# Kernel optimization log

Measured on AMD Instinct MI355X. Metric: run time of the kernel, lower is better.

## Reference

```python
import jax, jax.numpy as jnp
import numpy as np

B, S, DIN, DQ, DK = 8, 2048, 1024, 64, 64

def setup_inputs() -> dict:
    key = jax.random.key(0)
    ks = jax.random.split(key, 8)
    sc = 0.02
    return {
        "input_tensor": jax.random.normal(ks[0], (B, S, DIN), jnp.float32),
        "attention_mask": jax.random.randint(ks[1], (B, 1, S), 0, 2) == 1,
        "Wq": jax.random.normal(ks[2], (DIN, DQ), jnp.float32) * sc,
        "bq": jnp.zeros((DQ,), jnp.float32),
        "Wk": jax.random.normal(ks[3], (DIN, DK), jnp.float32) * sc,
        "bk": jnp.zeros((DK,), jnp.float32),
        "Wv": jax.random.normal(ks[4], (DIN, DK), jnp.float32) * sc,
        "bv": jnp.zeros((DK,), jnp.float32),
    }

def reference(input_tensor, attention_mask, Wq, bq, Wk, bk, Wv, bv):
    q = input_tensor @ Wq + bq          # [B,S,DQ]
    k = input_tensor @ Wk + bk          # [B,S,DK]
    v = input_tensor @ Wv + bv          # [B,S,DK]
    # NOTE: original scales by sqrt(query.size(1)) == sqrt(seq_len), faithfully kept
    scale = q.shape[1] ** 0.5
    scores = jnp.einsum('bqd,bkd->bqk', q, k) / scale
    scores = jnp.where(attention_mask, jnp.float32(-1e9), scores)
    attn = jax.nn.softmax(scores, axis=-1)
    context = jnp.einsum('bqk,bkd->bqd', attn, v)
    return context
```

## Files before the change

kernel.cpp:

```cpp
#include <hip/hip_runtime.h>
#include <hip/hip_bf16.h>

#define NB 8
#define SEQ 2048
#define DIN 1024
#define DH 64

typedef __attribute__((ext_vector_type(8))) short bf16x8;
typedef __attribute__((ext_vector_type(4))) float f32x4;

static __device__ __forceinline__ unsigned short f2bf(float f) {
    unsigned int u = __builtin_bit_cast(unsigned int, f);
    unsigned int r = (u + 0x7FFFu + ((u >> 16) & 1u)) >> 16;
    return (unsigned short)r;
}

static __device__ __forceinline__ unsigned int cvt_pk_bf16(float lo, float hi) {
    unsigned int d;
    asm volatile("v_cvt_pk_bf16_f32 %0, %1, %2" : "=v"(d) : "v"(lo), "v"(hi));
    return d;
}

__global__ __launch_bounds__(256) void prep_kernel(
    const float* __restrict__ Wq, const float* __restrict__ Wk, const float* __restrict__ Wv,
    unsigned short* __restrict__ Wfrag)
{
    int j = blockIdx.x * 256 + threadIdx.x;
    int mat = j >> 16;
    int rem = j & 65535;
    int k = rem >> 6;
    int c = rem & 63;
    const float* W = (mat == 0) ? Wq : ((mat == 1) ? Wk : Wv);
    float v = W[rem];
    int col = mat * 64 + c;
    int cg = col >> 4, cl = col & 15;
    int kk = k >> 5, kq = (k >> 3) & 3, ke = k & 7;
    Wfrag[(size_t)(cg * 32 + kk) * 512 + cl * 32 + kq * 8 + ke] = f2bf(v);
}

__global__ __launch_bounds__(256, 2) void qkv_kernel(
    const float* __restrict__ X, const unsigned short* __restrict__ Wfrag,
    const float* __restrict__ bq, const float* __restrict__ bk, const float* __restrict__ bv,
    unsigned short* __restrict__ Qb, unsigned short* __restrict__ Kb, unsigned short* __restrict__ Vt)
{
    __shared__ __align__(16) short As[2][32][128];

    const int tid = threadIdx.x;
    const int w   = tid >> 6;
    const int l15 = tid & 15;
    const int lq  = (tid >> 4) & 3;
    const int row0 = blockIdx.x * 32;

    f32x4 acc[2][3] = {};

    const float* xb = X + (size_t)row0 * DIN;

    const unsigned short* wfb[3];
    #pragma unroll
    for (int n = 0; n < 3; ++n)
        wfb[n] = Wfrag + (size_t)((w * 3 + n) * 32) * 512 + (l15 * 4 + lq) * 8;

    float4 pf[2][4];
    #pragma unroll
    for (int i = 0; i < 4; ++i) {
        int c = tid + 256 * i;
        const float* p = xb + (size_t)(c >> 5) * DIN + (c & 31) * 4;
        pf[0][i] = *(const float4*)(p);
        pf[1][i] = *(const float4*)(p + 128);
    }

    bf16x8 wb[6][3];
    #pragma unroll
    for (int s = 0; s < 6; ++s)
        #pragma unroll
        for (int n = 0; n < 3; ++n)
            wb[s][n] = *(const bf16x8*)(wfb[n] + (size_t)s * 512);

    #pragma unroll
    for (int step = 0; step < 8; ++step) {
        const int pi = step & 1;

        unsigned int u[8];
        #pragma unroll
        for (int i = 0; i < 4; ++i) {
            u[2 * i]     = cvt_pk_bf16(pf[pi][i].x, pf[pi][i].y);
            u[2 * i + 1] = cvt_pk_bf16(pf[pi][i].z, pf[pi][i].w);
        }
        #pragma unroll
        for (int i = 0; i < 4; ++i) {
            int c = tid + 256 * i;
            int r = c >> 5;
            int bo = ((c & 31) * 8) ^ ((r & 7) << 4);
            uint2 v2; v2.x = u[2 * i]; v2.y = u[2 * i + 1];
            *(uint2*)((char*)&As[pi][r][0] + bo) = v2;
        }
        if (step + 2 < 8) {
            #pragma unroll
            for (int i = 0; i < 4; ++i) {
                int c = tid + 256 * i;
                pf[pi][i] = *(const float4*)(xb + (size_t)(c >> 5) * DIN + (step + 2) * 128 + (c & 31) * 4);
            }
        }
        __syncthreads();

        #pragma unroll
        for (int kkl = 0; kkl < 4; ++kkl) {
            const int c = step * 4 + kkl;
            bf16x8 a[2];
            #pragma unroll
            for (int m = 0; m < 2; ++m) {
                int r = m * 16 + l15;
                int bo = ((kkl * 32 + lq * 8) * 2) ^ ((r & 7) << 4);
                a[m] = *(const bf16x8*)((const char*)&As[pi][r][0] + bo);
            }
            #pragma unroll
            for (int m = 0; m < 2; ++m)
                #pragma unroll
                for (int n = 0; n < 3; ++n)
                    acc[m][n] = __builtin_amdgcn_mfma_f32_16x16x32_bf16(a[m], wb[c % 6][n], acc[m][n], 0, 0, 0);
            if (c + 6 < 32) {
                #pragma unroll
                for (int n = 0; n < 3; ++n)
                    wb[c % 6][n] = *(const bf16x8*)(wfb[n] + (size_t)(c + 6) * 512);
            }
        }
    }

    #pragma unroll
    for (int n = 0; n < 3; ++n) {
        int col = w * 48 + n * 16 + l15;
        int mat = col >> 6, c = col & 63;
        float badd = ((mat == 0) ? bq : ((mat == 1) ? bk : bv))[c];
        #pragma unroll
        for (int m = 0; m < 2; ++m) {
            #pragma unroll
            for (int reg = 0; reg < 4; ++reg) {
                int row = row0 + m * 16 + lq * 4 + reg;
                unsigned short v16 = f2bf(acc[m][n][reg] + badd);
                if (mat == 0)      Qb[(size_t)row * DH + c] = v16;
                else if (mat == 1) Kb[(size_t)row * DH + c] = v16;
                else {
                    int bb = row >> 11, ss = row & 2047;
                    Vt[((size_t)(bb * DH + c)) * SEQ + ss] = v16;
                }
            }
        }
    }
}

#define AKT 64
#define ANT 8
#define PP 36

__global__ __launch_bounds__(256, 3) void attn_kernel(
    const unsigned short* __restrict__ Qb, const unsigned short* __restrict__ Kb,
    const unsigned short* __restrict__ Vt, const int* __restrict__ mask,
    float* __restrict__ Opart, float* __restrict__ lpart)
{
    __shared__ __align__(16) short Ks[2][AKT][DH];
    __shared__ __align__(16) short Vs[2][DH][AKT];
    __shared__ __align__(16) short ps[4][32][PP];
    __shared__ float sml[4][32];

    const int tid = threadIdx.x;
    const int w   = tid >> 6;
    const int l15 = tid & 15;
    const int lq  = (tid >> 4) & 3;
    const int wm  = w >> 1;
    const int wn  = w & 1;

    int bid = blockIdx.x;
    int sbid = (bid & 7) * 128 + (bid >> 3);
    const int b   = sbid >> 7;
    const int qt  = (sbid >> 2) & 31;
    const int kq  = sbid & 3;
    const int q0  = qt * 64;
    const int kb0 = kq * 512;

    bf16x8 aq[2][2];
    #pragma unroll
    for (int m = 0; m < 2; ++m)
        #pragma unroll
        for (int kk = 0; kk < 2; ++kk)
            aq[m][kk] = *(const bf16x8*)(Qb + ((size_t)(b * SEQ + q0 + wm * 32 + m * 16 + l15)) * DH + kk * 32 + lq * 8);

    const int srow = tid >> 3;
    const int scol = (tid & 7) * 8;
    const int sdst = scol ^ ((srow & 7) << 3);

    const unsigned short* Kst = Kb + ((size_t)(b * SEQ) + kb0 + srow) * DH + scol;
    const unsigned short* Vst = Vt + ((size_t)(b * DH) + srow) * SEQ + kb0 + scol;

    bf16x8 kr[2], vr[2];
    #pragma unroll
    for (int i = 0; i < 2; ++i) {
        kr[i] = *(const bf16x8*)(Kst + (size_t)(i * 32) * DH);
        vr[i] = *(const bf16x8*)(Vst + (size_t)(i * 32) * SEQ);
    }

    f32x4 o[2][4];
    #pragma unroll
    for (int m = 0; m < 2; ++m)
        #pragma unroll
        for (int n = 0; n < 4; ++n) o[m][n] = f32x4{0, 0, 0, 0};
    float lr[2][4] = {};

    const float rscale = 0.022097086912079612f;
    const int* mbase = mask + b * SEQ + kb0 + wn * 32 + l15;

    for (int t = 0; t < ANT; ++t) {
        const int cur = t & 1;

        #pragma unroll
        for (int i = 0; i < 2; ++i) *(bf16x8*)&Ks[cur][i * 32 + srow][sdst] = kr[i];
        #pragma unroll
        for (int i = 0; i < 2; ++i) *(bf16x8*)&Vs[cur][i * 32 + srow][sdst] = vr[i];

        int mk0 = mbase[t * AKT];
        int mk1 = mbase[t * AKT + 16];

        if (t + 1 < ANT) {
            #pragma unroll
            for (int i = 0; i < 2; ++i) {
                kr[i] = *(const bf16x8*)(Kst + (size_t)((t + 1) * AKT + i * 32) * DH);
                vr[i] = *(const bf16x8*)(Vst + (size_t)(i * 32) * SEQ + (t + 1) * AKT);
            }
        }

        __syncthreads();

        bf16x8 bkf[2][2];
        #pragma unroll
        for (int n = 0; n < 2; ++n)
            #pragma unroll
            for (int kk = 0; kk < 2; ++kk) {
                int row = wn * 32 + n * 16 + l15;
                bkf[n][kk] = *(const bf16x8*)&Ks[cur][row][(kk * 32 + lq * 8) ^ ((row & 7) << 3)];
            }
        f32x4 s[2][2];
        #pragma unroll
        for (int m = 0; m < 2; ++m)
            #pragma unroll
            for (int n = 0; n < 2; ++n) s[m][n] = f32x4{0, 0, 0, 0};
        #pragma unroll
        for (int kk = 0; kk < 2; ++kk)
            #pragma unroll
            for (int m = 0; m < 2; ++m)
                #pragma unroll
                for (int n = 0; n < 2; ++n)
                    s[m][n] = __builtin_amdgcn_mfma_f32_16x16x32_bf16(aq[m][kk], bkf[n][kk], s[m][n], 0, 0, 0);

        float bb0 = mk0 ? -1e30f : 0.0f;
        float bb1 = mk1 ? -1e30f : 0.0f;
        #pragma unroll
        for (int m = 0; m < 2; ++m)
            #pragma unroll
            for (int n = 0; n < 2; ++n) {
                float bvv = n ? bb1 : bb0;
                #pragma unroll
                for (int r = 0; r < 4; ++r) {
                    float p = __expf(fmaf(s[m][n][r], rscale, bvv));
                    lr[m][r] += p;
                    ps[w][m * 16 + lq * 4 + r][n * 16 + l15] = (short)f2bf(p);
                }
            }

        bf16x8 pa[2];
        #pragma unroll
        for (int m = 0; m < 2; ++m)
            pa[m] = *(const bf16x8*)&ps[w][m * 16 + l15][lq * 8];
        bf16x8 bvf[4];
        #pragma unroll
        for (int n = 0; n < 4; ++n) {
            int row = n * 16 + l15;
            bvf[n] = *(const bf16x8*)&Vs[cur][row][(wn * 32 + lq * 8) ^ ((row & 7) << 3)];
        }
        #pragma unroll
        for (int m = 0; m < 2; ++m)
            #pragma unroll
            for (int n = 0; n < 4; ++n)
                o[m][n] = __builtin_amdgcn_mfma_f32_16x16x32_bf16(pa[m], bvf[n], o[m][n], 0, 0, 0);
    }

    #pragma unroll
    for (int off = 1; off < 16; off <<= 1)
        #pragma unroll
        for (int m = 0; m < 2; ++m)
            #pragma unroll
            for (int r = 0; r < 4; ++r) lr[m][r] += __shfl_xor(lr[m][r], off);
    if (l15 == 0) {
        #pragma unroll
        for (int m = 0; m < 2; ++m)
            #pragma unroll
            for (int r = 0; r < 4; ++r) sml[w][m * 16 + lq * 4 + r] = lr[m][r];
    }
    __syncthreads();

    float (*mg)[32][64] = reinterpret_cast<float (*)[32][64]>(&Ks[0][0][0]);
    if (wn == 1) {
        #pragma unroll
        for (int m = 0; m < 2; ++m)
            #pragma unroll
            for (int n = 0; n < 4; ++n)
                #pragma unroll
                for (int r = 0; r < 4; ++r)
                    mg[wm][m * 16 + lq * 4 + r][n * 16 + l15] = o[m][n][r];
    }
    __syncthreads();
    if (wn == 0) {
        #pragma unroll
        for (int m = 0; m < 2; ++m)
            #pragma unroll
            for (int n = 0; n < 4; ++n)
                #pragma unroll
                for (int r = 0; r < 4; ++r)
                    mg[wm][m * 16 + lq * 4 + r][n * 16 + l15] += o[m][n][r];
    }
    __syncthreads();

    {
        int qq = tid >> 2;
        int d0 = (tid & 3) * 16;
        float* dst = Opart + ((size_t)kq * (NB * SEQ) + b * SEQ + q0 + qq) * DH + d0;
        #pragma unroll
        for (int j = 0; j < 4; ++j)
            *(float4*)(dst + j * 4) = *(float4*)&mg[qq >> 5][qq & 31][d0 + j * 4];
    }
    if (tid < 64) {
        int wmi = tid >> 5;
        float lsum = sml[wmi * 2][tid & 31] + sml[wmi * 2 + 1][tid & 31];
        lpart[(size_t)kq * (NB * SEQ) + b * SEQ + q0 + tid] = lsum;
    }
}

__global__ __launch_bounds__(256) void merge_kernel(
    const float* __restrict__ Opart, const float* __restrict__ lpart,
    float* __restrict__ out)
{
    int bid = blockIdx.x;
    int sbid = (bid & 7) * 32 + (bid >> 3);
    int g = sbid * 256 + threadIdx.x;
    int q  = g >> 2;
    int d0 = (g & 3) * 16;

    float l = lpart[q] + lpart[16384 + q] + lpart[2 * 16384 + q] + lpart[3 * 16384 + q];
    float inv = 1.0f / l;

    const float* o0 = Opart + (size_t)q * DH + d0;
    #pragma unroll
    for (int j = 0; j < 4; ++j) {
        float4 a = *(const float4*)(o0 + j * 4);
        float4 b2 = *(const float4*)(o0 + (size_t)16384 * DH + j * 4);
        float4 c = *(const float4*)(o0 + (size_t)2 * 16384 * DH + j * 4);
        float4 d = *(const float4*)(o0 + (size_t)3 * 16384 * DH + j * 4);
        float4 r;
        r.x = (a.x + b2.x + c.x + d.x) * inv;
        r.y = (a.y + b2.y + c.y + d.y) * inv;
        r.z = (a.z + b2.z + c.z + d.z) * inv;
        r.w = (a.w + b2.w + c.w + d.w) * inv;
        *(float4*)(out + (size_t)q * DH + d0 + j * 4) = r;
    }
}

extern "C" void kernel_launch(void* const* d_in, const int* in_sizes, int n_in,
                              void* d_out, int out_size, void* d_ws, size_t ws_size,
                              hipStream_t stream) {
    const float* X    = (const float*)d_in[0];
    const int*   mask = (const int*)d_in[1];
    const float* Wq   = (const float*)d_in[2];
    const float* bq   = (const float*)d_in[3];
    const float* Wk   = (const float*)d_in[4];
    const float* bk   = (const float*)d_in[5];
    const float* Wv   = (const float*)d_in[6];
    const float* bv   = (const float*)d_in[7];
    float* out = (float*)d_out;

    char* ws = (char*)d_ws;
    unsigned short* Qb    = (unsigned short*)(ws);
    unsigned short* Kb    = (unsigned short*)(ws + (2u << 20));
    unsigned short* Vt    = (unsigned short*)(ws + (4u << 20));
    unsigned short* Wfrag = (unsigned short*)(ws + (6u << 20));
    float* Opart          = (float*)(ws + (8u << 20));
    float* lpart          = (float*)(ws + (24u << 20));

    prep_kernel<<<768, 256, 0, stream>>>(Wq, Wk, Wv, Wfrag);
    qkv_kernel<<<512, 256, 0, stream>>>(X, Wfrag, bq, bk, bv, Qb, Kb, Vt);
    attn_kernel<<<1024, 256, 0, stream>>>(Qb, Kb, Vt, mask, Opart, lpart);
    merge_kernel<<<256, 256, 0, stream>>>(Opart, lpart, out);
}
```

Measured before the change: 61.08 us.

## Use direct global-to-LDS async loads with multi-stage buffering in QKV and attention kernels

Both the QKV projection and attention kernels now stage their inputs through LDS with global_load_lds, instead of register loads followed by LDS stores. Buffering is triple or double, synchronised with explicit vmcnt waits and raw barriers. QKV now stages fp32 X tiles and converts them to bf16 at fragment-read time, and the weight fragment layout is reordered so each k-step's weights are contiguous. The attention kernel preloads every mask value up front. The aim is to cut register pressure and copy instructions and to overlap memory with MFMA work. The cost is more LDS use (lower occupancy) and manual waitcnt accounting that must stay correct.

```diff
diff --git a/kernel.cpp b/kernel.cpp
--- a/kernel.cpp
+++ b/kernel.cpp
@@ -8,6 +8,7 @@
 
 typedef __attribute__((ext_vector_type(8))) short bf16x8;
 typedef __attribute__((ext_vector_type(4))) float f32x4;
+typedef __attribute__((ext_vector_type(4))) unsigned int u32x4;
 
 static __device__ __forceinline__ unsigned short f2bf(float f) {
     unsigned int u = __builtin_bit_cast(unsigned int, f);
@@ -20,6 +21,13 @@
     asm volatile("v_cvt_pk_bf16_f32 %0, %1, %2" : "=v"(d) : "v"(lo), "v"(hi));
     return d;
 }
+
+static __device__ __forceinline__ void gll16(const void* g, void* l) {
+    __builtin_amdgcn_global_load_lds((const __attribute__((address_space(1))) unsigned int*)g,
+                                     (__attribute__((address_space(3))) unsigned int*)l, 16, 0, 0);
+}
+
+#define WAITVM(N) asm volatile("s_waitcnt vmcnt(" #N ")" ::: "memory")
 
 __global__ __launch_bounds__(256) void prep_kernel(
     const float* __restrict__ Wq, const float* __restrict__ Wk, const float* __restrict__ Wv,
@@ -35,15 +43,16 @@
     int col = mat * 64 + c;
     int cg = col >> 4, cl = col & 15;
     int kk = k >> 5, kq = (k >> 3) & 3, ke = k & 7;
-    Wfrag[(size_t)(cg * 32 + kk) * 512 + cl * 32 + kq * 8 + ke] = f2bf(v);
-}
-
-__global__ __launch_bounds__(256, 2) void qkv_kernel(
+    Wfrag[(size_t)(kk * 12 + cg) * 512 + cl * 32 + kq * 8 + ke] = f2bf(v);
+}
+
+__global__ __launch_bounds__(256) void qkv_kernel(
     const float* __restrict__ X, const unsigned short* __restrict__ Wfrag,
     const float* __restrict__ bq, const float* __restrict__ bk, const float* __restrict__ bv,
     unsigned short* __restrict__ Qb, unsigned short* __restrict__ Kb, unsigned short* __restrict__ Vt)
 {
-    __shared__ __align__(16) short As[2][32][128];
+    __shared__ __align__(16) unsigned char Xs[3][8192];
+    __shared__ __align__(16) unsigned char Ws[2][24576];
 
     const int tid = threadIdx.x;
     const int w   = tid >> 6;
@@ -51,77 +60,69 @@
     const int lq  = (tid >> 4) & 3;
     const int row0 = blockIdx.x * 32;
 
+    const char* Xg = (const char*)(X + (size_t)row0 * DIN);
+    const char* Wg = (const char*)Wfrag;
+
+    int xlds[2], xsrc[2];
+    #pragma unroll
+    for (int i = 0; i < 2; ++i) {
+        int b = i * 4096 + tid * 16;
+        int row = b >> 8;
+        int g = (b >> 4) & 15;
+        xlds[i] = b;
+        xsrc[i] = row * 4096 + (g ^ (row & 7)) * 16;
+    }
+
     f32x4 acc[2][3] = {};
 
-    const float* xb = X + (size_t)row0 * DIN;
-
-    const unsigned short* wfb[3];
-    #pragma unroll
-    for (int n = 0; n < 3; ++n)
-        wfb[n] = Wfrag + (size_t)((w * 3 + n) * 32) * 512 + (l15 * 4 + lq) * 8;
-
-    float4 pf[2][4];
-    #pragma unroll
-    for (int i = 0; i < 4; ++i) {
-        int c = tid + 256 * i;
-        const float* p = xb + (size_t)(c >> 5) * DIN + (c & 31) * 4;
-        pf[0][i] = *(const float4*)(p);
-        pf[1][i] = *(const float4*)(p + 128);
-    }
-
-    bf16x8 wb[6][3];
-    #pragma unroll
-    for (int s = 0; s < 6; ++s)
-        #pragma unroll
-        for (int n = 0; n < 3; ++n)
-            wb[s][n] = *(const bf16x8*)(wfb[n] + (size_t)s * 512);
-
-    #pragma unroll
-    for (int step = 0; step < 8; ++step) {
-        const int pi = step & 1;
-
-        unsigned int u[8];
-        #pragma unroll
-        for (int i = 0; i < 4; ++i) {
-            u[2 * i]     = cvt_pk_bf16(pf[pi][i].x, pf[pi][i].y);
-            u[2 * i + 1] = cvt_pk_bf16(pf[pi][i].z, pf[pi][i].w);
-        }
-        #pragma unroll
-        for (int i = 0; i < 4; ++i) {
-            int c = tid + 256 * i;
-            int r = c >> 5;
-            int bo = ((c & 31) * 8) ^ ((r & 7) << 4);
-            uint2 v2; v2.x = u[2 * i]; v2.y = u[2 * i + 1];
-            *(uint2*)((char*)&As[pi][r][0] + bo) = v2;
-        }
-        if (step + 2 < 8) {
-            #pragma unroll
-            for (int i = 0; i < 4; ++i) {
-                int c = tid + 256 * i;
-                pf[pi][i] = *(const float4*)(xb + (size_t)(c >> 5) * DIN + (step + 2) * 128 + (c & 31) * 4);
+    #pragma unroll
+    for (int i = 0; i < 2; ++i) gll16(Xg + (size_t)xsrc[i], &Xs[0][xlds[i]]);
+    #pragma unroll
+    for (int i = 0; i < 6; ++i) gll16(Wg + (size_t)(i * 4096 + tid * 16), &Ws[0][i * 4096 + tid * 16]);
+    #pragma unroll
+    for (int i = 0; i < 2; ++i) gll16(Xg + (size_t)xsrc[i] + 256, &Xs[1][xlds[i]]);
+
+    #pragma unroll
+    for (int t = 0; t < 16; ++t) {
+        if (t < 15) { WAITVM(2); } else { WAITVM(0); }
+        __builtin_amdgcn_s_barrier();
+        __builtin_amdgcn_sched_barrier(0);
+
+        if (t + 1 < 16) {
+            #pragma unroll
+            for (int i = 0; i < 6; ++i)
+                gll16(Wg + (size_t)(t + 1) * 24576 + i * 4096 + tid * 16,
+                      &Ws[(t + 1) & 1][i * 4096 + tid * 16]);
+        }
+        if (t + 2 < 16) {
+            #pragma unroll
+            for (int i = 0; i < 2; ++i)
+                gll16(Xg + (size_t)xsrc[i] + (t + 2) * 256, &Xs[(t + 2) % 3][xlds[i]]);
+        }
+
+        const unsigned char* xb = Xs[t % 3];
+        const unsigned char* wt = Ws[t & 1];
+        #pragma unroll
+        for (int kk = 0; kk < 2; ++kk) {
+            bf16x8 a[2];
+            #pragma unroll
+            for (int m = 0; m < 2; ++m) {
+                int row = m * 16 + l15;
+                const unsigned char* rp = xb + row * 256;
+                f32x4 f0 = *(const f32x4*)(rp + ((kk * 8 + lq * 2 + 0) ^ (row & 7)) * 16);
+                f32x4 f1 = *(const f32x4*)(rp + ((kk * 8 + lq * 2 + 1) ^ (row & 7)) * 16);
+                u32x4 pk;
+                pk[0] = cvt_pk_bf16(f0[0], f0[1]);
+                pk[1] = cvt_pk_bf16(f0[2], f0[3]);
+                pk[2] = cvt_pk_bf16(f1[0], f1[1]);
+                pk[3] = cvt_pk_bf16(f1[2], f1[3]);
+                a[m] = __builtin_bit_cast(bf16x8, pk);
             }
-        }
-        __syncthreads();
-
-        #pragma unroll
-        for (int kkl = 0; kkl < 4; ++kkl) {
-            const int c = step * 4 + kkl;
-            bf16x8 a[2];
-            #pragma unroll
-            for (int m = 0; m < 2; ++m) {
-                int r = m * 16 + l15;
-                int bo = ((kkl * 32 + lq * 8) * 2) ^ ((r & 7) << 4);
-                a[m] = *(const bf16x8*)((const char*)&As[pi][r][0] + bo);
-            }
-            #pragma unroll
-            for (int m = 0; m < 2; ++m)
-                #pragma unroll
-                for (int n = 0; n < 3; ++n)
-                    acc[m][n] = __builtin_amdgcn_mfma_f32_16x16x32_bf16(a[m], wb[c % 6][n], acc[m][n], 0, 0, 0);
-            if (c + 6 < 32) {
-                #pragma unroll
-                for (int n = 0; n < 3; ++n)
-                    wb[c % 6][n] = *(const bf16x8*)(wfb[n] + (size_t)(c + 6) * 512);
+            #pragma unroll
+            for (int n = 0; n < 3; ++n) {
+                bf16x8 bf = *(const bf16x8*)(wt + (kk * 12 + w * 3 + n) * 1024 + (l15 * 4 + lq) * 16);
+                acc[0][n] = __builtin_amdgcn_mfma_f32_16x16x32_bf16(a[0], bf, acc[0][n], 0, 0, 0);
+                acc[1][n] = __builtin_amdgcn_mfma_f32_16x16x32_bf16(a[1], bf, acc[1][n], 0, 0, 0);
             }
         }
     }
@@ -152,14 +153,14 @@
 #define ANT 8
 #define PP 36
 
-__global__ __launch_bounds__(256, 3) void attn_kernel(
+__global__ __launch_bounds__(256) void attn_kernel(
     const unsigned short* __restrict__ Qb, const unsigned short* __restrict__ Kb,
     const unsigned short* __restrict__ Vt, const int* __restrict__ mask,
     float* __restrict__ Opart, float* __restrict__ lpart)
 {
-    __shared__ __align__(16) short Ks[2][AKT][DH];
-    __shared__ __align__(16) short Vs[2][DH][AKT];
-    __shared__ __align__(16) short ps[4][32][PP];
+    __shared__ __align__(16) unsigned char Ksm[3][8192];
+    __shared__ __align__(16) unsigned char Vsm[3][8192];
+    __shared__ short ps[4][32][PP];
     __shared__ float sml[4][32];
 
     const int tid = threadIdx.x;
@@ -184,18 +185,27 @@
         for (int kk = 0; kk < 2; ++kk)
             aq[m][kk] = *(const bf16x8*)(Qb + ((size_t)(b * SEQ + q0 + wm * 32 + m * 16 + l15)) * DH + kk * 32 + lq * 8);
 
-    const int srow = tid >> 3;
-    const int scol = (tid & 7) * 8;
-    const int sdst = scol ^ ((srow & 7) << 3);
-
-    const unsigned short* Kst = Kb + ((size_t)(b * SEQ) + kb0 + srow) * DH + scol;
-    const unsigned short* Vst = Vt + ((size_t)(b * DH) + srow) * SEQ + kb0 + scol;
-
-    bf16x8 kr[2], vr[2];
+    int mk[ANT][2];
+    #pragma unroll
+    for (int t = 0; t < ANT; ++t) {
+        mk[t][0] = mask[b * SEQ + kb0 + t * AKT + wn * 32 + l15];
+        mk[t][1] = mask[b * SEQ + kb0 + t * AKT + wn * 32 + 16 + l15];
+    }
+    WAITVM(0);
+
+    const char* Kg = (const char*)Kb + (size_t)(b * SEQ + kb0) * DH * 2;
+    const char* Vg = (const char*)Vt + ((size_t)(b * DH) * SEQ + kb0) * 2;
+
+    int slds[2], ksrc[2], vsrc[2];
     #pragma unroll
     for (int i = 0; i < 2; ++i) {
-        kr[i] = *(const bf16x8*)(Kst + (size_t)(i * 32) * DH);
-        vr[i] = *(const bf16x8*)(Vst + (size_t)(i * 32) * SEQ);
+        int bb = i * 4096 + tid * 16;
+        int row = bb >> 7;
+        int g = (bb >> 4) & 7;
+        int gs = g ^ (row & 7);
+        slds[i] = bb;
+        ksrc[i] = row * 128 + gs * 16;
+        vsrc[i] = row * 4096 + gs * 16;
     }
 
     f32x4 o[2][4];
@@ -204,30 +214,33 @@
         #pragma unroll
         for (int n = 0; n < 4; ++n) o[m][n] = f32x4{0, 0, 0, 0};
     float lr[2][4] = {};
-
     const float rscale = 0.022097086912079612f;
-    const int* mbase = mask + b * SEQ + kb0 + wn * 32 + l15;
-
+
+    #pragma unroll
+    for (int i = 0; i < 2; ++i) gll16(Kg + (size_t)ksrc[i], &Ksm[0][slds[i]]);
+    #pragma unroll
+    for (int i = 0; i < 2; ++i) gll16(Vg + (size_t)vsrc[i], &Vsm[0][slds[i]]);
+    #pragma unroll
+    for (int i = 0; i < 2; ++i) gll16(Kg + (size_t)8192 + ksrc[i], &Ksm[1][slds[i]]);
+    #pragma unroll
+    for (int i = 0; i < 2; ++i) gll16(Vg + (size_t)128 + vsrc[i], &Vsm[1][slds[i]]);
+
+    #pragma unroll
     for (int t = 0; t < ANT; ++t) {
-        const int cur = t & 1;
-
-        #pragma unroll
-        for (int i = 0; i < 2; ++i) *(bf16x8*)&Ks[cur][i * 32 + srow][sdst] = kr[i];
-        #pragma unroll
-        for (int i = 0; i < 2; ++i) *(bf16x8*)&Vs[cur][i * 32 + srow][sdst] = vr[i];
-
-        int mk0 = mbase[t * AKT];
-        int mk1 = mbase[t * AKT + 16];
-
-        if (t + 1 < ANT) {
-            #pragma unroll
-            for (int i = 0; i < 2; ++i) {
-                kr[i] = *(const bf16x8*)(Kst + (size_t)((t + 1) * AKT + i * 32) * DH);
-                vr[i] = *(const bf16x8*)(Vst + (size_t)(i * 32) * SEQ + (t + 1) * AKT);
-            }
-        }
-
-        __syncthreads();
+        if (t < ANT - 1) { WAITVM(4); } else { WAITVM(0); }
+        __builtin_amdgcn_s_barrier();
+        __builtin_amdgcn_sched_barrier(0);
+
+        if (t + 2 < ANT) {
+            int bi = (t + 2) % 3;
+            #pragma unroll
+            for (int i = 0; i < 2; ++i) gll16(Kg + (size_t)(t + 2) * 8192 + ksrc[i], &Ksm[bi][slds[i]]);
+            #pragma unroll
+            for (int i = 0; i < 2; ++i) gll16(Vg + (size_t)(t + 2) * 128 + vsrc[i], &Vsm[bi][slds[i]]);
+        }
+
+        const unsigned char* kt  = Ksm[t % 3];
+        const unsigned char* vt2 = Vsm[t % 3];
 
         bf16x8 bkf[2][2];
         #pragma unroll
@@ -235,7 +248,7 @@
             #pragma unroll
             for (int kk = 0; kk < 2; ++kk) {
                 int row = wn * 32 + n * 16 + l15;
-                bkf[n][kk] = *(const bf16x8*)&Ks[cur][row][(kk * 32 + lq * 8) ^ ((row & 7) << 3)];
+                bkf[n][kk] = *(const bf16x8*)(kt + row * 128 + ((4 * kk + lq) ^ (row & 7)) * 16);
             }
         f32x4 s[2][2];
         #pragma unroll
@@ -250,8 +263,8 @@
                 for (int n = 0; n < 2; ++n)
                     s[m][n] = __builtin_amdgcn_mfma_f32_16x16x32_bf16(aq[m][kk], bkf[n][kk], s[m][n], 0, 0, 0);
 
-        float bb0 = mk0 ? -1e30f : 0.0f;
-        float bb1 = mk1 ? -1e30f : 0.0f;
+        float bb0 = mk[t][0] ? -1e30f : 0.0f;
+        float bb1 = mk[t][1] ? -1e30f : 0.0f;
         #pragma unroll
         for (int m = 0; m < 2; ++m)
             #pragma unroll
@@ -273,7 +286,7 @@
         #pragma unroll
         for (int n = 0; n < 4; ++n) {
             int row = n * 16 + l15;
-            bvf[n] = *(const bf16x8*)&Vs[cur][row][(wn * 32 + lq * 8) ^ ((row & 7) << 3)];
+            bvf[n] = *(const bf16x8*)(vt2 + row * 128 + ((4 * wn + lq) ^ (row & 7)) * 16);
         }
         #pragma unroll
         for (int m = 0; m < 2; ++m)
@@ -296,7 +309,7 @@
     }
     __syncthreads();
 
-    float (*mg)[32][64] = reinterpret_cast<float (*)[32][64]>(&Ks[0][0][0]);
+    float (*mg)[32][64] = reinterpret_cast<float (*)[32][64]>(&Ksm[0][0]);
     if (wn == 1) {
         #pragma unroll
         for (int m = 0; m < 2; ++m)
```

New measurement: 62.41 us. 2.2% more time.
